# Kernel optimization log

Measured on AMD Instinct MI355X. Metric: run time of the kernel, lower is better.

Reference implementation:

```python
import jax, jax.numpy as jnp
import numpy as np

H, KVH, D, EPS = 8, 4, 64, 1e-5

def _rmsnorm(x, w):
    # normalize over last dim (head_dim)
    norm = jax.lax.rsqrt(jnp.mean(x * x, axis=-1, keepdims=True) + EPS)
    return x * norm * w

def setup_inputs() -> dict:
    key = jax.random.key(0)
    ks = jax.random.split(key, 5)
    B, S, Hid = 2048, 67, 512
    x = jax.random.normal(ks[0], (B, S, Hid), dtype=jnp.float32)
    # weights stored as [in, out] (equivalent to torch Linear weight.T)
    sc = 1.0 / np.sqrt(Hid)
    wq = jax.random.normal(ks[1], (Hid, H * D), dtype=jnp.float32) * sc
    wk = jax.random.normal(ks[2], (Hid, KVH * D), dtype=jnp.float32) * sc
    wv = jax.random.normal(ks[3], (Hid, KVH * D), dtype=jnp.float32) * sc
    wo = jax.random.normal(ks[4], (H * D, Hid), dtype=jnp.float32) * sc
    q_norm_w = jnp.ones((D,), dtype=jnp.float32)
    k_norm_w = jnp.ones((D,), dtype=jnp.float32)
    return {"x": x, "wq": wq, "wk": wk, "wv": wv, "wo": wo,
            "q_norm_w": q_norm_w, "k_norm_w": k_norm_w}

def reference(x, wq, wk, wv, wo, q_norm_w, k_norm_w):
    B, S, _ = x.shape
    G = H // KVH  # query heads per kv head
    q = (x @ wq).reshape(B, S, H, D).transpose(0, 2, 1, 3)      # (B,H,S,D)
    k = (x @ wk).reshape(B, S, KVH, D).transpose(0, 2, 1, 3)    # (B,KVH,S,D)
    v = (x @ wv).reshape(B, S, KVH, D).transpose(0, 2, 1, 3)
    q = _rmsnorm(q, q_norm_w)
    k = _rmsnorm(k, k_norm_w)
    qg = q.reshape(B, KVH, G, S, D)
    scale = 1.0 / np.sqrt(D)
    # bidirectional GQA attention, no mask
    scores = jnp.einsum('bkgsd,bktd->bkgst', qg, k) * scale      # (B,KVH,G,S,S)
    attn = jax.nn.softmax(scores, axis=-1)
    out = jnp.einsum('bkgst,bktd->bkgsd', attn, v)               # (B,KVH,G,S,D)
    out = out.reshape(B, H, S, D).transpose(0, 2, 1, 3).reshape(B, S, H * D)
    return out @ wo
```

## Files before the change

### kernel.cpp

```cpp
#include <hip/hip_runtime.h>
#include <hip/hip_bf16.h>

typedef __attribute__((ext_vector_type(8))) short short8;
typedef __attribute__((ext_vector_type(4))) float f32x4;

#define B_   2048
#define S_   67
#define M_   (B_*S_)
#define HID_ 512
#define H_   8
#define KVH_ 4
#define D_   64

__device__ __forceinline__ unsigned f2bf_u(float f){
  union { __hip_bfloat16 h; unsigned short u; } c; c.h = __float2bfloat16(f); return (unsigned)c.u;
}
__device__ __forceinline__ float bfu2f(unsigned u){
  union { unsigned short u; __hip_bfloat16 h; } c; c.u = (unsigned short)u; return __bfloat162float(c.h);
}
__device__ __forceinline__ unsigned pack2(float a, float b){ return f2bf_u(a) | (f2bf_u(b) << 16); }

__device__ __forceinline__ void unpack8(uint4 v, float* o){
  o[0]=bfu2f(v.x & 0xffffu); o[1]=bfu2f(v.x >> 16);
  o[2]=bfu2f(v.y & 0xffffu); o[3]=bfu2f(v.y >> 16);
  o[4]=bfu2f(v.z & 0xffffu); o[5]=bfu2f(v.z >> 16);
  o[6]=bfu2f(v.w & 0xffffu); o[7]=bfu2f(v.w >> 16);
}

union S8 { short8 v; unsigned short u[8]; };

__global__ __launch_bounds__(256) void prep_k(const float* __restrict__ x,
                                              const float* __restrict__ wq,
                                              const float* __restrict__ wk,
                                              const float* __restrict__ wv,
                                              const float* __restrict__ wo,
                                              unsigned short* __restrict__ xb,
                                              unsigned short* __restrict__ Wt,
                                              unsigned short* __restrict__ Wot){
  const int blk = blockIdx.x;
  if (blk < 768){
    __shared__ float tile[32][33];
    const float* src; unsigned short* dst; int ncols, row0, nb, kb;
    if (blk < 256)      { src = wq; dst = Wt;  ncols = 512; row0 = 0;
                          nb = (blk & 15)*32;        kb = (blk >> 4)*32; }
    else if (blk < 384) { int g = blk - 256; src = wk; dst = Wt; ncols = 256; row0 = 512;
                          nb = (g & 7)*32;           kb = (g >> 3)*32; }
    else if (blk < 512) { int g = blk - 384; src = wv; dst = Wt; ncols = 256; row0 = 768;
                          nb = (g & 7)*32;           kb = (g >> 3)*32; }
    else                { int g = blk - 512; src = wo; dst = Wot; ncols = 512; row0 = 0;
                          nb = (g & 15)*32;          kb = (g >> 4)*32; }
    const int tx = threadIdx.x & 31, ty = threadIdx.x >> 5;
    #pragma unroll
    for (int i = 0; i < 4; ++i){
      int r = ty + i*8;
      tile[r][tx] = src[(size_t)(kb + r)*ncols + nb + tx];
    }
    __syncthreads();
    #pragma unroll
    for (int i = 0; i < 4; ++i){
      int r = ty + i*8;
      dst[(size_t)(row0 + nb + r)*512 + kb + tx] = (unsigned short)f2bf_u(tile[tx][r]);
    }
  } else {
    long i = (long)(blk - 768)*256 + threadIdx.x;
    const float4 a = reinterpret_cast<const float4*>(x)[2*i];
    const float4 b = reinterpret_cast<const float4*>(x)[2*i+1];
    uint4 u = { pack2(a.x,a.y), pack2(a.z,a.w), pack2(b.x,b.y), pack2(b.z,b.w) };
    reinterpret_cast<uint4*>(xb)[i] = u;
  }
}

template<bool OUT_F32>
__global__ __launch_bounds__(512, 2) void gemm5_k(const unsigned short* __restrict__ A,
                                                  const unsigned short* __restrict__ Bw,
                                                  void* __restrict__ outp, int nbx){
  __shared__ unsigned short Sh[4][2][256*32];

  const int Nld = nbx << 8;
  const int per = gridDim.x >> 3;
  const int wg  = (blockIdx.x & 7) * per + (blockIdx.x >> 3);
  const int m0 = (wg / nbx) * 256;
  const int n0 = (wg % nbx) * 256;

  const int t = threadIdx.x;
  const int l = t & 63;
  const int w = t >> 6;
  const int wr = w >> 2, wc = w & 3;
  const int lr = l & 15, lk = l >> 4;

  const int srow  = w*16 + (l >> 2);
  const int skblk = (l & 3) ^ ((l >> 2) & 3) ^ ((l >> 4) & 3);
  const unsigned short* Ag0 = A  + (size_t)(m0 + srow)*512 + skblk*8;
  const unsigned short* Bg0 = Bw + (size_t)(n0 + srow)*512 + skblk*8;

  const int pk = (lk ^ (lr & 3) ^ ((lr >> 2) & 3)) * 8;

  f32x4 acc[8][4];
  #pragma unroll
  for (int f = 0; f < 8; ++f)
    #pragma unroll
    for (int g = 0; g < 4; ++g) acc[f][g] = (f32x4){0.f, 0.f, 0.f, 0.f};

  short8 bv[4];

#define STAGE_OP_(op_, kt_) do{ \
    const unsigned short* src_ = ((op_) ? Bg0 : Ag0) + (size_t)(kt_)*32; \
    unsigned short* dst_ = &Sh[(kt_)&3][op_][(w*16)*32]; \
    __builtin_amdgcn_global_load_lds((const unsigned int*)src_, (unsigned int*)dst_, 16, 0, 0); \
    __builtin_amdgcn_global_load_lds((const unsigned int*)(src_ + (size_t)128*512), \
                                     (unsigned int*)(dst_ + 128*32), 16, 0, 0); \
  }while(0)

#define PHASE_(kt_, q_) do{ \
    const unsigned short* Asl = &Sh[(kt_)&3][0][0]; \
    const unsigned short* Bsl = &Sh[(kt_)&3][1][0]; \
    short8 av[4]; \
    _Pragma("unroll") \
    for (int f2 = 0; f2 < 4; ++f2) \
      av[f2] = *reinterpret_cast<const short8*>(Asl + (wr*128 + ((q_)*4 + f2)*16 + lr)*32 + pk); \
    if ((q_) == 0){ \
      _Pragma("unroll") \
      for (int g = 0; g < 4; ++g) \
        bv[g] = *reinterpret_cast<const short8*>(Bsl + (wc*64 + g*16 + lr)*32 + pk); \
    } \
    if ((kt_) + 2 <= 15) STAGE_OP_((q_), (kt_) + 2); \
    __builtin_amdgcn_s_barrier(); \
    asm volatile("s_waitcnt lgkmcnt(0)" ::: "memory"); \
    __builtin_amdgcn_sched_barrier(0); \
    __builtin_amdgcn_s_setprio(1); \
    _Pragma("unroll") \
    for (int f2 = 0; f2 < 4; ++f2) \
      _Pragma("unroll") \
      for (int g = 0; g < 4; ++g) \
        acc[(q_)*4 + f2][g] = __builtin_amdgcn_mfma_f32_16x16x32_bf16(av[f2], bv[g], acc[(q_)*4 + f2][g], 0, 0, 0); \
    __builtin_amdgcn_s_setprio(0); \
    if ((q_) == 1){ \
      if ((kt_) < 14)       { asm volatile("s_waitcnt vmcnt(4)" ::: "memory"); } \
      else if ((kt_) == 14) { asm volatile("s_waitcnt vmcnt(0)" ::: "memory"); } \
      __builtin_amdgcn_sched_barrier(0); \
    } \
    __builtin_amdgcn_s_barrier(); \
  }while(0)

  STAGE_OP_(0, 0); STAGE_OP_(1, 0); STAGE_OP_(0, 1); STAGE_OP_(1, 1);
  asm volatile("s_waitcnt vmcnt(4)" ::: "memory");
  __builtin_amdgcn_sched_barrier(0);
  __builtin_amdgcn_s_barrier();

  #pragma unroll
  for (int kt = 0; kt < 16; ++kt){
    PHASE_(kt, 0);
    PHASE_(kt, 1);
  }
#undef PHASE_
#undef STAGE_OP_

  if (OUT_F32){
    float* Cs = reinterpret_cast<float*>(&Sh[0][0][0]);
    float* out = (float*)outp;
    #pragma unroll
    for (int half = 0; half < 2; ++half){
      __syncthreads();
      if (wr == half){
        #pragma unroll
        for (int f = 0; f < 8; ++f)
          #pragma unroll
          for (int g = 0; g < 4; ++g)
            #pragma unroll
            for (int r = 0; r < 4; ++r){
              int row = f*16 + lk*4 + r;
              int col = wc*64 + g*16 + lr;
              Cs[row*256 + col] = acc[f][g][r];
            }
      }
      __syncthreads();
      const float4* Cv = reinterpret_cast<const float4*>(Cs);
      #pragma unroll
      for (int p = 0; p < 16; ++p){
        int idx = p*512 + t;
        int row = idx >> 6, c4 = idx & 63;
        *reinterpret_cast<float4*>(out + (size_t)(m0 + half*128 + row)*Nld + n0 + c4*4) = Cv[idx];
      }
    }
  } else {
    unsigned short* Cs = &Sh[0][0][0];
    unsigned short* out = (unsigned short*)outp;
    #pragma unroll
    for (int half = 0; half < 2; ++half){
      __syncthreads();
      if (wr == half){
        #pragma unroll
        for (int f = 0; f < 8; ++f)
          #pragma unroll
          for (int g = 0; g < 4; ++g)
            #pragma unroll
            for (int r = 0; r < 4; ++r){
              int row = f*16 + lk*4 + r;
              int col = wc*64 + g*16 + lr;
              Cs[row*256 + col] = (unsigned short)f2bf_u(acc[f][g][r]);
            }
      }
      __syncthreads();
      const uint4* Cv = reinterpret_cast<const uint4*>(Cs);
      #pragma unroll
      for (int p = 0; p < 8; ++p){
        int idx = p*512 + t;
        int row = idx >> 5, c16 = idx & 31;
        *reinterpret_cast<uint4*>(out + (size_t)(m0 + half*128 + row)*Nld + n0 + c16*8) = Cv[idx];
      }
    }
  }
}

__global__ __launch_bounds__(576, 7) void attn_k(const unsigned short* __restrict__ qkv,
                                                 const float* __restrict__ qnw,
                                                 const float* __restrict__ knw,
                                                 unsigned short* __restrict__ attn){
  __shared__ unsigned short Vt[64*104];
  __shared__ unsigned short Kf[5][2][64*8];
  __shared__ unsigned short Pb[9][16*104];
  const int t = threadIdx.x;
  const int b = blockIdx.x >> 2, kvh = blockIdx.x & 3;
  const size_t rowbase = (size_t)b * 67;
  const int l = t & 63, w = t >> 6;
  const int lr = l & 15, lk = l >> 4;

  const int vs = t >> 3, vd0 = (t & 7) << 3;
  uint4 vu = {0u,0u,0u,0u};
  if (vs < 67)
    vu = *reinterpret_cast<const uint4*>(qkv + (rowbase + vs)*1024 + 768 + kvh*64 + vd0);
  uint4 ku0 = {0u,0u,0u,0u}, ku1 = {0u,0u,0u,0u};
  if (w < 5){
    int s = w*16 + lr; if (s > 66) s = 66;
    const unsigned short* kp = qkv + (rowbase + s)*1024 + 512 + kvh*64 + lk*8;
    ku0 = *reinterpret_cast<const uint4*>(kp);
    ku1 = *reinterpret_cast<const uint4*>(kp + 32);
  }
  const int qrow = w*16 + lr;
  const int h01 = (qrow >= 67) ? 1 : 0;
  int qr = qrow - (h01 ? 67 : 0); if (qr > 66) qr = 66;
  const unsigned short* qp = qkv + (rowbase + qr)*1024 + (kvh*2 + h01)*64 + lk*8;
  const uint4 qu0 = *reinterpret_cast<const uint4*>(qp);
  const uint4 qu1 = *reinterpret_cast<const uint4*>(qp + 32);

  {
    unsigned short vsv[8];
    vsv[0]=vu.x&0xffffu; vsv[1]=vu.x>>16; vsv[2]=vu.y&0xffffu; vsv[3]=vu.y>>16;
    vsv[4]=vu.z&0xffffu; vsv[5]=vu.z>>16; vsv[6]=vu.w&0xffffu; vsv[7]=vu.w>>16;
    const int slot = vs >> 3;
    #pragma unroll
    for (int j = 0; j < 8; ++j){
      int d = vd0 + j;
      int phys = slot ^ ((d >> 3) & 3);
      Vt[d*104 + phys*8 + (vs & 7)] = vsv[j];
    }
    if (t < 192){
      int s2 = 72 + (t >> 3);
      int slot2 = s2 >> 3;
      #pragma unroll
      for (int j = 0; j < 8; ++j){
        int d = vd0 + j;
        int phys = slot2 ^ ((d >> 3) & 3);
        Vt[d*104 + phys*8 + (s2 & 7)] = 0;
      }
    }
  }

  if (w < 5){
    float wp[16];
    #pragma unroll
    for (int hh = 0; hh < 2; ++hh)
      #pragma unroll
      for (int j = 0; j < 8; ++j){
        int idx = hh*32 + lk*8 + j;
        wp[hh*8+j] = qnw[idx] * knw[idx] * 0.125f;
      }
    float f[16]; unpack8(ku0, f); unpack8(ku1, f + 8);
    float ss = 0.f;
    #pragma unroll
    for (int j = 0; j < 16; ++j) ss += f[j]*f[j];
    ss += __shfl_xor(ss, 16); ss += __shfl_xor(ss, 32);
    float inv = rsqrtf(ss*(1.0f/64.0f) + 1e-5f);
    S8 a0, a1;
    #pragma unroll
    for (int j = 0; j < 8; ++j){
      a0.u[j] = (unsigned short)f2bf_u(f[j]   * inv * wp[j]);
      a1.u[j] = (unsigned short)f2bf_u(f[8+j] * inv * wp[8+j]);
    }
    *reinterpret_cast<short8*>(&Kf[w][0][l*8]) = a0.v;
    *reinterpret_cast<short8*>(&Kf[w][1][l*8]) = a1.v;
  }

  short8 qf0, qf1;
  {
    float f[16]; unpack8(qu0, f); unpack8(qu1, f + 8);
    float ss = 0.f;
    #pragma unroll
    for (int j = 0; j < 16; ++j) ss += f[j]*f[j];
    ss += __shfl_xor(ss, 16); ss += __shfl_xor(ss, 32);
    float inv = rsqrtf(ss*(1.0f/64.0f) + 1e-5f);
    S8 a0, a1;
    #pragma unroll
    for (int j = 0; j < 8; ++j){
      a0.u[j] = (unsigned short)f2bf_u(f[j]   * inv);
      a1.u[j] = (unsigned short)f2bf_u(f[8+j] * inv);
    }
    qf0 = a0.v; qf1 = a1.v;
  }

  {
    uint4 z = {0u,0u,0u,0u};
    uint4* pz = reinterpret_cast<uint4*>(Pb[w]);
    for (int i = l; i < 208; i += 64) pz[i] = z;
  }
  __syncthreads();

  f32x4 sa[5];
  #pragma unroll
  for (int nt = 0; nt < 5; ++nt){
    short8 k0 = *reinterpret_cast<const short8*>(&Kf[nt][0][l*8]);
    short8 k1 = *reinterpret_cast<const short8*>(&Kf[nt][1][l*8]);
    sa[nt] = (f32x4){0.f,0.f,0.f,0.f};
    sa[nt] = __builtin_amdgcn_mfma_f32_16x16x32_bf16(qf0, k0, sa[nt], 0,0,0);
    sa[nt] = __builtin_amdgcn_mfma_f32_16x16x32_bf16(qf1, k1, sa[nt], 0,0,0);
  }

  float inv4[4];
  #pragma unroll
  for (int r = 0; r < 4; ++r){
    float mx = -1e30f;
    #pragma unroll
    for (int nt = 0; nt < 5; ++nt){
      float v = sa[nt][r];
      if (nt*16 + lr >= 67) v = -1e30f;
      sa[nt][r] = v; mx = fmaxf(mx, v);
    }
    mx = fmaxf(mx, __shfl_xor(mx, 1));
    mx = fmaxf(mx, __shfl_xor(mx, 2));
    mx = fmaxf(mx, __shfl_xor(mx, 4));
    mx = fmaxf(mx, __shfl_xor(mx, 8));
    float sm = 0.f;
    #pragma unroll
    for (int nt = 0; nt < 5; ++nt){
      float e = __expf(sa[nt][r] - mx);
      sa[nt][r] = e; sm += e;
    }
    sm += __shfl_xor(sm, 1);
    sm += __shfl_xor(sm, 2);
    sm += __shfl_xor(sm, 4);
    sm += __shfl_xor(sm, 8);
    inv4[r] = 1.0f / sm;
  }

  unsigned short* pb = Pb[w];
  #pragma unroll
  for (int nt = 0; nt < 5; ++nt)
    #pragma unroll
    for (int r = 0; r < 4; ++r){
      int row = lk*4 + r, col = nt*16 + lr;
      int phys = (col >> 3) ^ ((row >> 3) & 3);
      pb[row*104 + phys*8 + (col & 7)] = (unsigned short)f2bf_u(sa[nt][r]);
    }

  f32x4 oa[4];
  #pragma unroll
  for (int dt = 0; dt < 4; ++dt) oa[dt] = (f32x4){0.f,0.f,0.f,0.f};
  #pragma unroll
  for (int ks = 0; ks < 3; ++ks){
    int physp = (ks*4 + lk) ^ ((lr >> 3) & 3);
    short8 pf = *reinterpret_cast<const short8*>(&pb[lr*104 + physp*8]);
    #pragma unroll
    for (int dt = 0; dt < 4; ++dt){
      int d = dt*16 + lr;
      int physv = (ks*4 + lk) ^ ((d >> 3) & 3);
      short8 vf = *reinterpret_cast<const short8*>(&Vt[d*104 + physv*8]);
      oa[dt] = __builtin_amdgcn_mfma_f32_16x16x32_bf16(pf, vf, oa[dt], 0,0,0);
    }
  }

  #pragma unroll
  for (int dt = 0; dt < 4; ++dt)
    #pragma unroll
    for (int r = 0; r < 4; ++r){
      int row = w*16 + lk*4 + r;
      if (row < 134){
        int hh = (row >= 67) ? 1 : 0;
        int orow = row - (hh ? 67 : 0);
        attn[(rowbase + orow)*512 + (kvh*2 + hh)*64 + dt*16 + lr] =
            (unsigned short)f2bf_u(oa[dt][r] * inv4[r]);
      }
    }
}

extern "C" void kernel_launch(void* const* d_in, const int* in_sizes, int n_in,
                              void* d_out, int out_size, void* d_ws, size_t ws_size,
                              hipStream_t stream){
  const float* x   = (const float*)d_in[0];
  const float* wq  = (const float*)d_in[1];
  const float* wk  = (const float*)d_in[2];
  const float* wv  = (const float*)d_in[3];
  const float* wo  = (const float*)d_in[4];
  const float* qnw = (const float*)d_in[5];
  const float* knw = (const float*)d_in[6];

  unsigned short* Wt   = (unsigned short*)d_ws;
  unsigned short* Wot  = Wt + 1024*512;
  unsigned short* qkv  = Wot + 512*512;
  unsigned short* attn = qkv + (size_t)M_*1024;
  unsigned short* xb   = attn;

  prep_k<<<dim3(768 + M_*512/8/256), 256, 0, stream>>>(x, wq, wk, wv, wo, xb, Wt, Wot);

  gemm5_k<false><<<dim3(4 * (M_/256)), 512, 0, stream>>>(xb, Wt, qkv, 4);

  attn_k<<<dim3(B_*KVH_), 576, 0, stream>>>(qkv, qnw, knw, attn);

  gemm5_k<true><<<dim3(2 * (M_/256)), 512, 0, stream>>>(attn, Wot, d_out, 2);
}
```

Before: 514.5 us.

## Load GEMM B operand straight to registers and double-buffer A in LDS

The GEMM kernel now loads the weight (B) fragments from global memory directly into registers, one k-step ahead, instead of staging them through LDS. Only the activation (A) tiles go through LDS, using a two-stage buffer instead of four stages. This halves the shared-memory footprint, which is meant to let two workgroups fit per CU and to cut LDS traffic. The fp32 epilogue is split into quarters to fit the smaller buffer. The cost is that global-load latency for B now sits closer to the MFMA loop, with a shallower prefetch.

```diff
diff --git a/kernel.cpp b/kernel.cpp
--- a/kernel.cpp
+++ b/kernel.cpp
@@ -71,10 +71,10 @@
 }
 
 template<bool OUT_F32>
-__global__ __launch_bounds__(512, 2) void gemm5_k(const unsigned short* __restrict__ A,
+__global__ __launch_bounds__(512, 2) void gemm7_k(const unsigned short* __restrict__ A,
                                                   const unsigned short* __restrict__ Bw,
                                                   void* __restrict__ outp, int nbx){
-  __shared__ unsigned short Sh[4][2][256*32];
+  __shared__ unsigned short Sh[4][256*32];
 
   const int Nld = nbx << 8;
   const int per = gridDim.x >> 3;
@@ -90,8 +90,9 @@
 
   const int srow  = w*16 + (l >> 2);
   const int skblk = (l & 3) ^ ((l >> 2) & 3) ^ ((l >> 4) & 3);
-  const unsigned short* Ag0 = A  + (size_t)(m0 + srow)*512 + skblk*8;
-  const unsigned short* Bg0 = Bw + (size_t)(n0 + srow)*512 + skblk*8;
+  const unsigned short* Ag0 = A + (size_t)(m0 + srow)*512 + skblk*8;
+
+  const unsigned short* Bgl = Bw + (size_t)(n0 + wc*64 + lr)*512 + lk*8;
 
   const int pk = (lk ^ (lr & 3) ^ ((lr >> 2) & 3)) * 8;
 
@@ -101,89 +102,86 @@
     #pragma unroll
     for (int g = 0; g < 4; ++g) acc[f][g] = (f32x4){0.f, 0.f, 0.f, 0.f};
 
-  short8 bv[4];
-
-#define STAGE_OP_(op_, kt_) do{ \
-    const unsigned short* src_ = ((op_) ? Bg0 : Ag0) + (size_t)(kt_)*32; \
-    unsigned short* dst_ = &Sh[(kt_)&3][op_][(w*16)*32]; \
+  short8 bvv[2][4];
+
+#define STAGE_A_(kt_) do{ \
+    const unsigned short* src_ = Ag0 + (size_t)(kt_)*32; \
+    unsigned short* dst_ = &Sh[(kt_)&1][(w*16)*32]; \
     __builtin_amdgcn_global_load_lds((const unsigned int*)src_, (unsigned int*)dst_, 16, 0, 0); \
     __builtin_amdgcn_global_load_lds((const unsigned int*)(src_ + (size_t)128*512), \
                                      (unsigned int*)(dst_ + 128*32), 16, 0, 0); \
   }while(0)
 
-#define PHASE_(kt_, q_) do{ \
-    const unsigned short* Asl = &Sh[(kt_)&3][0][0]; \
-    const unsigned short* Bsl = &Sh[(kt_)&3][1][0]; \
-    short8 av[4]; \
+#define LOADB_(kt_) do{ \
     _Pragma("unroll") \
-    for (int f2 = 0; f2 < 4; ++f2) \
-      av[f2] = *reinterpret_cast<const short8*>(Asl + (wr*128 + ((q_)*4 + f2)*16 + lr)*32 + pk); \
-    if ((q_) == 0){ \
-      _Pragma("unroll") \
-      for (int g = 0; g < 4; ++g) \
-        bv[g] = *reinterpret_cast<const short8*>(Bsl + (wc*64 + g*16 + lr)*32 + pk); \
-    } \
-    if ((kt_) + 2 <= 15) STAGE_OP_((q_), (kt_) + 2); \
-    __builtin_amdgcn_s_barrier(); \
-    asm volatile("s_waitcnt lgkmcnt(0)" ::: "memory"); \
-    __builtin_amdgcn_sched_barrier(0); \
-    __builtin_amdgcn_s_setprio(1); \
-    _Pragma("unroll") \
-    for (int f2 = 0; f2 < 4; ++f2) \
-      _Pragma("unroll") \
-      for (int g = 0; g < 4; ++g) \
-        acc[(q_)*4 + f2][g] = __builtin_amdgcn_mfma_f32_16x16x32_bf16(av[f2], bv[g], acc[(q_)*4 + f2][g], 0, 0, 0); \
-    __builtin_amdgcn_s_setprio(0); \
-    if ((q_) == 1){ \
-      if ((kt_) < 14)       { asm volatile("s_waitcnt vmcnt(4)" ::: "memory"); } \
-      else if ((kt_) == 14) { asm volatile("s_waitcnt vmcnt(0)" ::: "memory"); } \
-      __builtin_amdgcn_sched_barrier(0); \
-    } \
-    __builtin_amdgcn_s_barrier(); \
+    for (int g = 0; g < 4; ++g) \
+      bvv[(kt_)&1][g] = *reinterpret_cast<const short8*>(Bgl + (size_t)g*8192 + (kt_)*32); \
   }while(0)
 
-  STAGE_OP_(0, 0); STAGE_OP_(1, 0); STAGE_OP_(0, 1); STAGE_OP_(1, 1);
-  asm volatile("s_waitcnt vmcnt(4)" ::: "memory");
+  STAGE_A_(0);
+  LOADB_(0);
+  asm volatile("s_waitcnt vmcnt(0)" ::: "memory");
   __builtin_amdgcn_sched_barrier(0);
-  __builtin_amdgcn_s_barrier();
 
   #pragma unroll
   for (int kt = 0; kt < 16; ++kt){
-    PHASE_(kt, 0);
-    PHASE_(kt, 1);
-  }
-#undef PHASE_
-#undef STAGE_OP_
+    if (kt < 15){ STAGE_A_(kt + 1); LOADB_(kt + 1); }
+    if (kt < 15) asm volatile("s_waitcnt vmcnt(6)" ::: "memory");
+    else         asm volatile("s_waitcnt vmcnt(0)" ::: "memory");
+    __builtin_amdgcn_sched_barrier(0);
+    __builtin_amdgcn_s_barrier();
+    __builtin_amdgcn_sched_barrier(0);
+
+    const unsigned short* As = &Sh[kt&1][0];
+    short8 av[8];
+    #pragma unroll
+    for (int f = 0; f < 8; ++f)
+      av[f] = *reinterpret_cast<const short8*>(As + (wr*128 + f*16 + lr)*32 + pk);
+    __builtin_amdgcn_s_setprio(1);
+    #pragma unroll
+    for (int f = 0; f < 8; ++f)
+      #pragma unroll
+      for (int g = 0; g < 4; ++g)
+        acc[f][g] = __builtin_amdgcn_mfma_f32_16x16x32_bf16(av[f], bvv[kt&1][g], acc[f][g], 0, 0, 0);
+    __builtin_amdgcn_s_setprio(0);
+    asm volatile("s_waitcnt lgkmcnt(0)" ::: "memory");
+    __builtin_amdgcn_sched_barrier(0);
+    __builtin_amdgcn_s_barrier();
+  }
+#undef STAGE_A_
+#undef LOADB_
 
   if (OUT_F32){
-    float* Cs = reinterpret_cast<float*>(&Sh[0][0][0]);
+    float* Cs = reinterpret_cast<float*>(&Sh[0][0]);
     float* out = (float*)outp;
     #pragma unroll
-    for (int half = 0; half < 2; ++half){
+    for (int qq = 0; qq < 4; ++qq){
       __syncthreads();
-      if (wr == half){
+      if (wr == (qq >> 1)){
         #pragma unroll
-        for (int f = 0; f < 8; ++f)
+        for (int f2 = 0; f2 < 4; ++f2){
+          int f = (qq & 1)*4 + f2;
           #pragma unroll
           for (int g = 0; g < 4; ++g)
             #pragma unroll
             for (int r = 0; r < 4; ++r){
-              int row = f*16 + lk*4 + r;
+              int row = f2*16 + lk*4 + r;
               int col = wc*64 + g*16 + lr;
               Cs[row*256 + col] = acc[f][g][r];
             }
+        }
       }
       __syncthreads();
       const float4* Cv = reinterpret_cast<const float4*>(Cs);
       #pragma unroll
-      for (int p = 0; p < 16; ++p){
+      for (int p = 0; p < 8; ++p){
         int idx = p*512 + t;
         int row = idx >> 6, c4 = idx & 63;
-        *reinterpret_cast<float4*>(out + (size_t)(m0 + half*128 + row)*Nld + n0 + c4*4) = Cv[idx];
+        *reinterpret_cast<float4*>(out + (size_t)(m0 + qq*64 + row)*Nld + n0 + c4*4) = Cv[idx];
       }
     }
   } else {
-    unsigned short* Cs = &Sh[0][0][0];
+    unsigned short* Cs = &Sh[0][0];
     unsigned short* out = (unsigned short*)outp;
     #pragma unroll
     for (int half = 0; half < 2; ++half){
@@ -411,9 +409,9 @@
 
   prep_k<<<dim3(768 + M_*512/8/256), 256, 0, stream>>>(x, wq, wk, wv, wo, xb, Wt, Wot);
 
-  gemm5_k<false><<<dim3(4 * (M_/256)), 512, 0, stream>>>(xb, Wt, qkv, 4);
+  gemm7_k<false><<<dim3(4 * (M_/256)), 512, 0, stream>>>(xb, Wt, qkv, 4);
 
   attn_k<<<dim3(B_*KVH_), 576, 0, stream>>>(qkv, qnw, knw, attn);
 
-  gemm5_k<true><<<dim3(2 * (M_/256)), 512, 0, stream>>>(attn, Wot, d_out, 2);
-}
+  gemm7_k<true><<<dim3(2 * (M_/256)), 512, 0, stream>>>(attn, Wot, d_out, 2);
+}
```

New measurement: 663.3 us. +28.9%, slower.
